# Performance work log

Hardware: AMD Instinct MI355X
Metric: run time of the kernel (lower is better)

Reference implementation:

```python
import jax, jax.numpy as jnp
import numpy as np

B, S, D_MODEL, N_HEADS, D_K, D_V = 2, 2048, 1024, 16, 64, 64


def setup_inputs() -> dict:
    key = jax.random.key(0)
    k1, k2, k3, k4, k5, k6, k7 = jax.random.split(key, 7)
    scale = 1.0 / np.sqrt(D_MODEL)
    inputs = {
        "input_Q": jax.random.normal(k1, (B, S, D_MODEL), dtype=jnp.float32),
        "input_K": jax.random.normal(k2, (B, S, D_MODEL), dtype=jnp.float32),
        "input_V": jax.random.normal(k3, (B, S, D_MODEL), dtype=jnp.float32),
        # causal mask: True means position is masked out (matches masked_fill_)
        "attn_mask": jnp.broadcast_to(
            ~jnp.tril(jnp.ones((S, S), dtype=bool)), (B, S, S)
        ),
        "flag": 0,
        "W_Q": jax.random.normal(k4, (D_MODEL, N_HEADS * D_K), dtype=jnp.float32) * scale,
        "W_K": jax.random.normal(k5, (D_MODEL, N_HEADS * D_K), dtype=jnp.float32) * scale,
        "W_V": jax.random.normal(k6, (D_MODEL, N_HEADS * D_V), dtype=jnp.float32) * scale,
        "W_O": jax.random.normal(k7, (N_HEADS * D_V, D_MODEL), dtype=jnp.float32) * scale,
    }
    return inputs


def reference(input_Q, input_K, input_V, attn_mask, flag, W_Q, W_K, W_V, W_O):
    b = input_Q.shape[0]
    # project and split heads: [b, h, s, d]
    Q = (input_Q @ W_Q).reshape(b, -1, N_HEADS, D_K).transpose(0, 2, 1, 3)
    K = (input_K @ W_K).reshape(b, -1, N_HEADS, D_K).transpose(0, 2, 1, 3)
    V = (input_V @ W_V).reshape(b, -1, N_HEADS, D_V).transpose(0, 2, 1, 3)
    # scaled dot-product attention with additive large-negative masking
    scores = jnp.einsum("bhqd,bhkd->bhqk", Q, K) / np.sqrt(D_K).astype(np.float32)
    scores = jnp.where(attn_mask[:, None, :, :], jnp.float32(-1e9), scores)
    attn = jax.nn.softmax(scores, axis=-1)
    context = jnp.einsum("bhqk,bhkd->bhqd", attn, V)  # [b, h, s, d_v]
    context = context.transpose(0, 2, 1, 3).reshape(b, -1, N_HEADS * D_V)
    return context @ W_O
```

## Files before the change

kernel.cpp:

```cpp
#include <hip/hip_runtime.h>

#define DEVINL __device__ __forceinline__

typedef __attribute__((ext_vector_type(8))) short short8;
typedef __attribute__((ext_vector_type(4))) short sh4;
typedef __attribute__((ext_vector_type(4))) float floatx4;

constexpr int S_LEN = 2048;
constexpr int DM    = 1024;
constexpr int NHEAD = 16;
constexpr int DHEAD = 64;
constexpr int BATCH = 2;
constexpr int MROWS = BATCH * S_LEN;
constexpr float LOG2E = 1.44269504f;
constexpr float SM_C1 = 0.125f * LOG2E;
constexpr float SM_C2 = -24.0f * LOG2E;

#define MFMA16(a, b, c) __builtin_amdgcn_mfma_f32_16x16x16bf16_1k(a, b, c, 0, 0, 0)

DEVINL unsigned short f2bf(float x) {
  union { float f; unsigned u; } un; un.f = x;
  unsigned u = un.u;
  return (unsigned short)((u + 0x7fffu + ((u >> 16) & 1u)) >> 16);
}
DEVINL unsigned short f2bf_fast(float x) {
  union { float f; unsigned u; } un; un.f = x;
  return (unsigned short)((un.u + 0x8000u) >> 16);
}

__global__ __launch_bounds__(256) void prep_kernel(const float* __restrict__ s0,
                                                   const float* __restrict__ s1,
                                                   const float* __restrict__ s2,
                                                   unsigned short* __restrict__ d0,
                                                   unsigned short* __restrict__ d1,
                                                   unsigned short* __restrict__ d2,
                                                   const float* __restrict__ W0,
                                                   const float* __restrict__ W1,
                                                   const float* __restrict__ W2,
                                                   const float* __restrict__ W3,
                                                   unsigned short* __restrict__ T0,
                                                   unsigned short* __restrict__ T1,
                                                   unsigned short* __restrict__ T2,
                                                   unsigned short* __restrict__ T3) {
  __shared__ unsigned short tile[32][33];
  const int y = blockIdx.y;
  if (y < 3) {
    const float* s = y == 0 ? s0 : (y == 1 ? s1 : s2);
    unsigned short* d = y == 0 ? d0 : (y == 1 ? d1 : d2);
    int i = (blockIdx.x * 256 + threadIdx.x) * 4;
    float4 v = *(const float4*)(s + i);
    unsigned lo = (unsigned)f2bf(v.x) | ((unsigned)f2bf(v.y) << 16);
    unsigned hi = (unsigned)f2bf(v.z) | ((unsigned)f2bf(v.w) << 16);
    *(uint2*)(d + i) = make_uint2(lo, hi);
  } else {
    const int x = blockIdx.x;
    const int wsel = x >> 10, rem = x & 1023;
    const float* W = wsel == 0 ? W0 : (wsel == 1 ? W1 : (wsel == 2 ? W2 : W3));
    unsigned short* Wt = wsel == 0 ? T0 : (wsel == 1 ? T1 : (wsel == 2 ? T2 : T3));
    int t = threadIdx.x;
    int c = t & 31, r0 = t >> 5;
    int nB = (rem & 31) * 32, kB = (rem >> 5) * 32;
    for (int i = 0; i < 4; ++i) {
      int r = r0 + i * 8;
      tile[r][c] = f2bf(W[(size_t)(kB + r) * DM + nB + c]);
    }
    __syncthreads();
    for (int i = 0; i < 4; ++i) {
      int r = r0 + i * 8;
      Wt[(size_t)(nB + r) * DM + kB + c] = tile[c][r];
    }
  }
}

DEVINL void load_lds16(const unsigned short* g, unsigned short* l) {
  __builtin_amdgcn_global_load_lds((const __attribute__((address_space(1))) unsigned int*)g,
                                   (__attribute__((address_space(3))) unsigned int*)l,
                                   16, 0, 0);
}

template <int MODE>
DEVINL void gemm_body(const unsigned short* __restrict__ A,
                      const unsigned short* __restrict__ Bt,
                      void* __restrict__ Cout) {
  constexpr int K = 1024, N = 1024;
  __shared__ alignas(16) unsigned short As[128 * 32];
  __shared__ alignas(16) unsigned short Bs[128 * 32];
  const int tid  = threadIdx.x;
  const int wave = tid >> 6, lane = tid & 63;
  const int quad = lane >> 4, l16 = lane & 15;
  const int mBase = blockIdx.y * 128, nBase = blockIdx.x * 128;
  const int wm = (wave >> 1) * 64, wn = (wave & 1) * 64;
  const int sr = lane >> 2;
  const int sc = (lane & 3) * 8;
  floatx4 acc[4][4] = {};

  for (int k0 = 0; k0 < K; k0 += 32) {
    __syncthreads();
#pragma unroll
    for (int j = 0; j < 2; ++j) {
      int row = wave * 32 + j * 16 + sr;
      load_lds16(A  + (size_t)(mBase + row) * K + k0 + sc, As + (wave * 32 + j * 16) * 32);
      load_lds16(Bt + (size_t)(nBase + row) * K + k0 + sc, Bs + (wave * 32 + j * 16) * 32);
    }
    __syncthreads();
    short8 af[4], bfr[4];
#pragma unroll
    for (int mt = 0; mt < 4; ++mt) af[mt]  = *(const short8*)&As[(wm + mt * 16 + l16) * 32 + quad * 8];
#pragma unroll
    for (int nt = 0; nt < 4; ++nt) bfr[nt] = *(const short8*)&Bs[(wn + nt * 16 + l16) * 32 + quad * 8];
#pragma unroll
    for (int mt = 0; mt < 4; ++mt)
#pragma unroll
      for (int nt = 0; nt < 4; ++nt)
        acc[mt][nt] = __builtin_amdgcn_mfma_f32_16x16x32_bf16(af[mt], bfr[nt], acc[mt][nt], 0, 0, 0);
  }

#pragma unroll
  for (int mt = 0; mt < 4; ++mt)
#pragma unroll
    for (int nt = 0; nt < 4; ++nt) {
      const int m = mBase + wm + mt * 16 + quad * 4;
      const int n = nBase + wn + nt * 16 + l16;
      if (MODE == 2) {
        const int bq = m >> 11, s = m & 2047;
        const int hh = n >> 6,  d = n & 63;
        unsigned short w4[4];
#pragma unroll
        for (int r = 0; r < 4; ++r) w4[r] = f2bf(acc[mt][nt][r]);
        *(uint2*)&((unsigned short*)Cout)[((size_t)((bq * 16 + hh) * 64 + d)) * S_LEN + s] =
            *(const uint2*)w4;
      } else {
#pragma unroll
        for (int r = 0; r < 4; ++r)
          ((unsigned short*)Cout)[(size_t)(m + r) * N + n] = f2bf(acc[mt][nt][r]);
      }
    }
}

__global__ __launch_bounds__(256) void gemm_qkv(const unsigned short* __restrict__ A0,
                                                const unsigned short* __restrict__ A1,
                                                const unsigned short* __restrict__ A2,
                                                const unsigned short* __restrict__ B0,
                                                const unsigned short* __restrict__ B1,
                                                const unsigned short* __restrict__ B2,
                                                unsigned short* __restrict__ C0,
                                                unsigned short* __restrict__ C1,
                                                unsigned short* __restrict__ C2) {
  const int z = blockIdx.z;
  if (z == 2)      gemm_body<2>(A2, B2, C2);
  else if (z == 1) gemm_body<0>(A1, B1, C1);
  else             gemm_body<0>(A0, B0, C0);
}

__global__ __launch_bounds__(256) void gemm_out64(const unsigned short* __restrict__ A,
                                                  const unsigned short* __restrict__ Bt,
                                                  float* __restrict__ C) {
  constexpr int K = 1024, N = 1024;
  __shared__ alignas(16) unsigned short As[64 * 32];
  __shared__ alignas(16) unsigned short Bs[128 * 32];
  const int tid  = threadIdx.x;
  const int wave = tid >> 6, lane = tid & 63;
  const int quad = lane >> 4, l16 = lane & 15;
  const int mBase = blockIdx.y * 64, nBase = blockIdx.x * 128;
  const int wm = (wave >> 1) * 32, wn = (wave & 1) * 64;
  const int sr = lane >> 2;
  const int sc = (lane & 3) * 8;
  floatx4 acc[2][4] = {};

  for (int k0 = 0; k0 < K; k0 += 32) {
    __syncthreads();
    load_lds16(A + (size_t)(mBase + wave * 16 + sr) * K + k0 + sc, As + (wave * 16) * 32);
#pragma unroll
    for (int j = 0; j < 2; ++j) {
      int row = wave * 32 + j * 16 + sr;
      load_lds16(Bt + (size_t)(nBase + row) * K + k0 + sc, Bs + (wave * 32 + j * 16) * 32);
    }
    __syncthreads();
    short8 af[2], bfr[4];
#pragma unroll
    for (int mt = 0; mt < 2; ++mt) af[mt]  = *(const short8*)&As[(wm + mt * 16 + l16) * 32 + quad * 8];
#pragma unroll
    for (int nt = 0; nt < 4; ++nt) bfr[nt] = *(const short8*)&Bs[(wn + nt * 16 + l16) * 32 + quad * 8];
#pragma unroll
    for (int mt = 0; mt < 2; ++mt)
#pragma unroll
      for (int nt = 0; nt < 4; ++nt)
        acc[mt][nt] = __builtin_amdgcn_mfma_f32_16x16x32_bf16(af[mt], bfr[nt], acc[mt][nt], 0, 0, 0);
  }

#pragma unroll
  for (int mt = 0; mt < 2; ++mt)
#pragma unroll
    for (int nt = 0; nt < 4; ++nt)
#pragma unroll
      for (int r = 0; r < 4; ++r) {
        int m = mBase + wm + mt * 16 + quad * 4 + r;
        int n = nBase + wn + nt * 16 + l16;
        C[(size_t)m * N + n] = acc[mt][nt][r];
      }
}

__global__ __launch_bounds__(256, 3) void attn_kernel(const unsigned short* __restrict__ Qp,
                                                      const unsigned short* __restrict__ Kp,
                                                      const unsigned short* __restrict__ Vtg,
                                                      unsigned short* __restrict__ ctx) {
  const int bh = blockIdx.y;
  const int b  = bh >> 4, h = bh & 15;
  const int tid = threadIdx.x;
  const int w = tid >> 6, lane = tid & 63;
  const int quad = lane >> 4, l16 = lane & 15;

  __shared__ alignas(16) unsigned short KVs[2 * 8192];
  __shared__ float rsL[4][4][16];
  __shared__ alignas(16) float Ored[4][4][16][20];

  const unsigned short* Kbh = Kp  + (size_t)(b * S_LEN) * DM + h * DHEAD;
  const unsigned short* Vbh = Vtg + (size_t)(bh * DHEAD) * S_LEN;

  int srow[4], scol[4];
#pragma unroll
  for (int j = 0; j < 4; ++j) {
    const int p = (w & 1) * 256 + j * 64 + lane;
    srow[j] = p >> 3;
    scol[j] = ((p & 7) ^ (srow[j] & 7)) * 8;
  }
  const bool stageK = (w < 2);

  const int swz = l16 & 7;
  const int kRow = (w * 16 + l16) * 64;
  const int kOff0 = kRow + ((0 + quad) ^ swz) * 8;
  const int kOff1 = kRow + ((4 + quad) ^ swz) * 8;
  int vOff[4];
#pragma unroll
  for (int dt = 0; dt < 4; ++dt) {
    const int ch = 2 * w + (quad >> 1);
    vOff[dt] = 4096 + (dt * 16 + l16) * 64 + (ch ^ swz) * 8 + (quad & 1) * 4;
  }

  {
    unsigned short* dst = KVs + w * 2048;
#pragma unroll
    for (int j = 0; j < 4; ++j) {
      const unsigned short* src = stageK
          ? Kbh + (size_t)srow[j] * DM + scol[j]
          : Vbh + (size_t)srow[j] * S_LEN + scol[j];
      load_lds16(src, dst + j * 512);
    }
  }

  int cur = 0;

#pragma unroll 1
  for (int half = 0; half < 2; ++half) {
    const int qt = half ? (int)blockIdx.x : 31 - (int)blockIdx.x;
    const int Q0 = qt * 64;
    const int nT = qt + 1;

    short8 qB[4][2];
#pragma unroll
    for (int nt = 0; nt < 4; ++nt) {
      const size_t qr = ((size_t)(b * S_LEN + Q0 + nt * 16 + l16)) * DM + h * DHEAD + quad * 8;
      qB[nt][0] = *(const short8*)&Qp[qr];
      qB[nt][1] = *(const short8*)&Qp[qr + 32];
    }

    floatx4 o[4][4] = {};
    float rs[4] = {0.f, 0.f, 0.f, 0.f};

#pragma unroll 1
    for (int t = 0; t < nT; ++t) {
      asm volatile("s_waitcnt vmcnt(0)" ::: "memory");
      __syncthreads();

      const unsigned short* buf = KVs + cur * 8192;
      short8 kc0 = *(const short8*)&buf[kOff0];
      short8 kc1 = *(const short8*)&buf[kOff1];
      sh4 vv[4];
#pragma unroll
      for (int dt = 0; dt < 4; ++dt) vv[dt] = *(const sh4*)&buf[vOff[dt]];

      {
        const int tn = (t + 1 < nT) ? t + 1 : 0;
        const int kb = tn * 64;
        unsigned short* dst = KVs + (cur ^ 1) * 8192 + w * 2048;
#pragma unroll
        for (int j = 0; j < 4; ++j) {
          const unsigned short* src = stageK
              ? Kbh + (size_t)(kb + srow[j]) * DM + scol[j]
              : Vbh + (size_t)srow[j] * S_LEN + kb + scol[j];
          load_lds16(src, dst + j * 512);
        }
      }

      const bool masked = (t == nT - 1);
      const int sbase = w * 16 + quad * 4;

#pragma unroll
      for (int nt = 0; nt < 4; ++nt) {
        floatx4 sc = {};
        sc = __builtin_amdgcn_mfma_f32_16x16x32_bf16(kc0, qB[nt][0], sc, 0, 0, 0);
        sc = __builtin_amdgcn_mfma_f32_16x16x32_bf16(kc1, qB[nt][1], sc, 0, 0, 0);
        const int qoff = nt * 16 + l16;
        sh4 pa;
        float acc = 0.f;
#pragma unroll
        for (int r = 0; r < 4; ++r) {
          float p = __builtin_amdgcn_exp2f(fmaf(sc[r], SM_C1, SM_C2));
          if (masked && (sbase + r > qoff)) p = 0.f;
          acc += p;
          pa[r] = (short)f2bf_fast(p);
        }
        rs[nt] += acc;
#pragma unroll
        for (int dt = 0; dt < 4; ++dt)
          o[nt][dt] = MFMA16(pa, vv[dt], o[nt][dt]);
      }

      cur ^= 1;
    }

#pragma unroll
    for (int nt = 0; nt < 4; ++nt) {
      rs[nt] += __shfl_xor(rs[nt], 16, 64);
      rs[nt] += __shfl_xor(rs[nt], 32, 64);
    }
    if (quad == 0) {
#pragma unroll
      for (int nt = 0; nt < 4; ++nt) rsL[w][nt][l16] = rs[nt];
    }

    for (int nt = 0; nt < 4; ++nt) {
      __syncthreads();
#pragma unroll
      for (int dt = 0; dt < 4; ++dt)
        *(floatx4*)&Ored[w][dt][l16][quad * 4] = o[nt][dt];
      __syncthreads();
      floatx4 acc = {};
#pragma unroll
      for (int w2 = 0; w2 < 4; ++w2) {
        floatx4 v = *(const floatx4*)&Ored[w2][w][l16][quad * 4];
#pragma unroll
        for (int j = 0; j < 4; ++j) acc[j] += v[j];
      }
#pragma unroll
      for (int j = 0; j < 4; ++j) {
        const int q16 = quad * 4 + j;
        float l = rsL[0][nt][q16] + rsL[1][nt][q16] + rsL[2][nt][q16] + rsL[3][nt][q16];
        const size_t row = (size_t)(b * S_LEN + Q0 + nt * 16 + q16);
        ctx[row * DM + h * DHEAD + w * 16 + l16] = f2bf(acc[j] / l);
      }
    }
  }
}

extern "C" void kernel_launch(void* const* d_in, const int* in_sizes, int n_in,
                              void* d_out, int out_size, void* d_ws, size_t ws_size,
                              hipStream_t stream) {
  const float* Xq = (const float*)d_in[0];
  const float* Xk = (const float*)d_in[1];
  const float* Xv = (const float*)d_in[2];
  const float* Wq = (const float*)d_in[5];
  const float* Wk = (const float*)d_in[6];
  const float* Wv = (const float*)d_in[7];
  const float* Wo = (const float*)d_in[8];
  float* out = (float*)d_out;

  char* ws = (char*)d_ws;
  constexpr size_t XBYTES = (size_t)MROWS * DM * 2;
  constexpr size_t WBYTES = (size_t)DM * DM * 2;
  unsigned short* xq_bf = (unsigned short*)(ws);
  unsigned short* xk_bf = (unsigned short*)(ws + XBYTES);
  unsigned short* xv_bf = (unsigned short*)(ws + 2 * XBYTES);
  unsigned short* wqt   = (unsigned short*)(ws + 3 * XBYTES);
  unsigned short* wkt   = (unsigned short*)(ws + 3 * XBYTES + WBYTES);
  unsigned short* wvt   = (unsigned short*)(ws + 3 * XBYTES + 2 * WBYTES);
  unsigned short* wot   = (unsigned short*)(ws + 3 * XBYTES + 3 * WBYTES);
  unsigned short* qp    = (unsigned short*)(ws + 3 * XBYTES + 4 * WBYTES);
  unsigned short* kp    = (unsigned short*)(ws + 4 * XBYTES + 4 * WBYTES);
  unsigned short* vt    = (unsigned short*)(ws + 5 * XBYTES + 4 * WBYTES);
  unsigned short* ctx   = xq_bf;

  prep_kernel<<<dim3(4096, 4), 256, 0, stream>>>(Xq, Xk, Xv, xq_bf, xk_bf, xv_bf,
                                                 Wq, Wk, Wv, Wo, wqt, wkt, wvt, wot);

  gemm_qkv<<<dim3(DM / 128, MROWS / 128, 3), 256, 0, stream>>>(
      xq_bf, xk_bf, xv_bf, wqt, wkt, wvt, qp, kp, vt);

  attn_kernel<<<dim3(16, BATCH * NHEAD), 256, 0, stream>>>(qp, kp, vt, ctx);

  gemm_out64<<<dim3(DM / 128, MROWS / 64), 256, 0, stream>>>(ctx, wot, out);
}
```

Before: 231.3 us.

## Split attention query tiles across two wave groups with 512-thread blocks

The attention kernel moves to 512 threads. Waves are split into 4 key-slice groups times 2 query groups, so each wave holds half the output accumulators and Q fragments, and K/V staging is spread across all 8 waves. The LDS buffers are unioned so the reduction scratch reuses the K/V buffer, and the prefetch of the next half's first tile is replaced by a restart per half. The aim is fewer registers per wave and more waves to hide latency, at the cost of an extra sync and lost cross-half prefetch overlap.

```diff
diff --git a/kernel.cpp b/kernel.cpp
--- a/kernel.cpp
+++ b/kernel.cpp
@@ -200,7 +200,7 @@
       }
 }
 
-__global__ __launch_bounds__(256, 3) void attn_kernel(const unsigned short* __restrict__ Qp,
+__global__ __launch_bounds__(512, 4) void attn_kernel(const unsigned short* __restrict__ Qp,
                                                       const unsigned short* __restrict__ Kp,
                                                       const unsigned short* __restrict__ Vtg,
                                                       unsigned short* __restrict__ ctx) {
@@ -209,46 +209,37 @@
   const int tid = threadIdx.x;
   const int w = tid >> 6, lane = tid & 63;
   const int quad = lane >> 4, l16 = lane & 15;
-
-  __shared__ alignas(16) unsigned short KVs[2 * 8192];
-  __shared__ float rsL[4][4][16];
-  __shared__ alignas(16) float Ored[4][4][16][20];
+  const int sgrp = w & 3, qgrp = w >> 2;
+
+  __shared__ alignas(16) char smem[41984];
+  unsigned short* KVs = (unsigned short*)smem;
+  float* OredB = (float*)smem;
+  float* rsLB  = (float*)(smem + 40960);
 
   const unsigned short* Kbh = Kp  + (size_t)(b * S_LEN) * DM + h * DHEAD;
   const unsigned short* Vbh = Vtg + (size_t)(bh * DHEAD) * S_LEN;
 
-  int srow[4], scol[4];
-#pragma unroll
-  for (int j = 0; j < 4; ++j) {
-    const int p = (w & 1) * 256 + j * 64 + lane;
+  const bool stageK = (w < 4);
+  const int vbase = stageK ? 0 : 4096;
+  int srow[2], scol[2];
+#pragma unroll
+  for (int j = 0; j < 2; ++j) {
+    const int p = sgrp * 128 + j * 64 + lane;
     srow[j] = p >> 3;
     scol[j] = ((p & 7) ^ (srow[j] & 7)) * 8;
   }
-  const bool stageK = (w < 2);
+  const int dstOff = vbase + sgrp * 1024;
 
   const int swz = l16 & 7;
-  const int kRow = (w * 16 + l16) * 64;
+  const int kRow = (sgrp * 16 + l16) * 64;
   const int kOff0 = kRow + ((0 + quad) ^ swz) * 8;
   const int kOff1 = kRow + ((4 + quad) ^ swz) * 8;
   int vOff[4];
 #pragma unroll
   for (int dt = 0; dt < 4; ++dt) {
-    const int ch = 2 * w + (quad >> 1);
+    const int ch = 2 * sgrp + (quad >> 1);
     vOff[dt] = 4096 + (dt * 16 + l16) * 64 + (ch ^ swz) * 8 + (quad & 1) * 4;
   }
-
-  {
-    unsigned short* dst = KVs + w * 2048;
-#pragma unroll
-    for (int j = 0; j < 4; ++j) {
-      const unsigned short* src = stageK
-          ? Kbh + (size_t)srow[j] * DM + scol[j]
-          : Vbh + (size_t)srow[j] * S_LEN + scol[j];
-      load_lds16(src, dst + j * 512);
-    }
-  }
-
-  int cur = 0;
 
 #pragma unroll 1
   for (int half = 0; half < 2; ++half) {
@@ -256,16 +247,30 @@
     const int Q0 = qt * 64;
     const int nT = qt + 1;
 
-    short8 qB[4][2];
-#pragma unroll
-    for (int nt = 0; nt < 4; ++nt) {
+    __syncthreads();
+    int cur = 0;
+    {
+      unsigned short* dst = KVs + dstOff;
+#pragma unroll
+      for (int j = 0; j < 2; ++j) {
+        const unsigned short* src = stageK
+            ? Kbh + (size_t)srow[j] * DM + scol[j]
+            : Vbh + (size_t)srow[j] * S_LEN + scol[j];
+        load_lds16(src, dst + j * 512);
+      }
+    }
+
+    short8 qB[2][2];
+#pragma unroll
+    for (int ntl = 0; ntl < 2; ++ntl) {
+      const int nt = qgrp * 2 + ntl;
       const size_t qr = ((size_t)(b * S_LEN + Q0 + nt * 16 + l16)) * DM + h * DHEAD + quad * 8;
-      qB[nt][0] = *(const short8*)&Qp[qr];
-      qB[nt][1] = *(const short8*)&Qp[qr + 32];
-    }
-
-    floatx4 o[4][4] = {};
-    float rs[4] = {0.f, 0.f, 0.f, 0.f};
+      qB[ntl][0] = *(const short8*)&Qp[qr];
+      qB[ntl][1] = *(const short8*)&Qp[qr + 32];
+    }
+
+    floatx4 o[2][4] = {};
+    float rs[2] = {0.f, 0.f};
 
 #pragma unroll 1
     for (int t = 0; t < nT; ++t) {
@@ -279,12 +284,11 @@
 #pragma unroll
       for (int dt = 0; dt < 4; ++dt) vv[dt] = *(const sh4*)&buf[vOff[dt]];
 
-      {
-        const int tn = (t + 1 < nT) ? t + 1 : 0;
-        const int kb = tn * 64;
-        unsigned short* dst = KVs + (cur ^ 1) * 8192 + w * 2048;
-#pragma unroll
-        for (int j = 0; j < 4; ++j) {
+      if (t + 1 < nT) {
+        const int kb = (t + 1) * 64;
+        unsigned short* dst = KVs + (cur ^ 1) * 8192 + dstOff;
+#pragma unroll
+        for (int j = 0; j < 2; ++j) {
           const unsigned short* src = stageK
               ? Kbh + (size_t)(kb + srow[j]) * DM + scol[j]
               : Vbh + (size_t)srow[j] * S_LEN + kb + scol[j];
@@ -293,13 +297,14 @@
       }
 
       const bool masked = (t == nT - 1);
-      const int sbase = w * 16 + quad * 4;
-
-#pragma unroll
-      for (int nt = 0; nt < 4; ++nt) {
+      const int sbase = sgrp * 16 + quad * 4;
+
+#pragma unroll
+      for (int ntl = 0; ntl < 2; ++ntl) {
+        const int nt = qgrp * 2 + ntl;
         floatx4 sc = {};
-        sc = __builtin_amdgcn_mfma_f32_16x16x32_bf16(kc0, qB[nt][0], sc, 0, 0, 0);
-        sc = __builtin_amdgcn_mfma_f32_16x16x32_bf16(kc1, qB[nt][1], sc, 0, 0, 0);
+        sc = __builtin_amdgcn_mfma_f32_16x16x32_bf16(kc0, qB[ntl][0], sc, 0, 0, 0);
+        sc = __builtin_amdgcn_mfma_f32_16x16x32_bf16(kc1, qB[ntl][1], sc, 0, 0, 0);
         const int qoff = nt * 16 + l16;
         sh4 pa;
         float acc = 0.f;
@@ -310,44 +315,50 @@
           acc += p;
           pa[r] = (short)f2bf_fast(p);
         }
-        rs[nt] += acc;
+        rs[ntl] += acc;
 #pragma unroll
         for (int dt = 0; dt < 4; ++dt)
-          o[nt][dt] = MFMA16(pa, vv[dt], o[nt][dt]);
+          o[ntl][dt] = MFMA16(pa, vv[dt], o[ntl][dt]);
       }
 
       cur ^= 1;
     }
 
 #pragma unroll
-    for (int nt = 0; nt < 4; ++nt) {
-      rs[nt] += __shfl_xor(rs[nt], 16, 64);
-      rs[nt] += __shfl_xor(rs[nt], 32, 64);
+    for (int ntl = 0; ntl < 2; ++ntl) {
+      rs[ntl] += __shfl_xor(rs[ntl], 16, 64);
+      rs[ntl] += __shfl_xor(rs[ntl], 32, 64);
     }
     if (quad == 0) {
 #pragma unroll
-      for (int nt = 0; nt < 4; ++nt) rsL[w][nt][l16] = rs[nt];
-    }
-
-    for (int nt = 0; nt < 4; ++nt) {
+      for (int ntl = 0; ntl < 2; ++ntl) rsLB[(w * 2 + ntl) * 16 + l16] = rs[ntl];
+    }
+
+#pragma unroll 1
+    for (int ntl = 0; ntl < 2; ++ntl) {
+      const int nt = qgrp * 2 + ntl;
       __syncthreads();
 #pragma unroll
       for (int dt = 0; dt < 4; ++dt)
-        *(floatx4*)&Ored[w][dt][l16][quad * 4] = o[nt][dt];
+        *(floatx4*)&OredB[((((qgrp * 4 + sgrp) * 4 + dt) * 16 + l16) * 20) + quad * 4] =
+            o[ntl][dt];
       __syncthreads();
       floatx4 acc = {};
 #pragma unroll
-      for (int w2 = 0; w2 < 4; ++w2) {
-        floatx4 v = *(const floatx4*)&Ored[w2][w][l16][quad * 4];
+      for (int s2 = 0; s2 < 4; ++s2) {
+        floatx4 v = *(const floatx4*)&OredB[((((qgrp * 4 + s2) * 4 + sgrp) * 16 + l16) * 20) + quad * 4];
 #pragma unroll
         for (int j = 0; j < 4; ++j) acc[j] += v[j];
       }
 #pragma unroll
       for (int j = 0; j < 4; ++j) {
         const int q16 = quad * 4 + j;
-        float l = rsL[0][nt][q16] + rsL[1][nt][q16] + rsL[2][nt][q16] + rsL[3][nt][q16];
+        float l = rsLB[((qgrp * 4 + 0) * 2 + ntl) * 16 + q16] +
+                  rsLB[((qgrp * 4 + 1) * 2 + ntl) * 16 + q16] +
+                  rsLB[((qgrp * 4 + 2) * 2 + ntl) * 16 + q16] +
+                  rsLB[((qgrp * 4 + 3) * 2 + ntl) * 16 + q16];
         const size_t row = (size_t)(b * S_LEN + Q0 + nt * 16 + q16);
-        ctx[row * DM + h * DHEAD + w * 16 + l16] = f2bf(acc[j] / l);
+        ctx[row * DM + h * DHEAD + sgrp * 16 + l16] = f2bf(acc[j] / l);
       }
     }
   }
@@ -386,7 +397,7 @@
   gemm_qkv<<<dim3(DM / 128, MROWS / 128, 3), 256, 0, stream>>>(
       xq_bf, xk_bf, xv_bf, wqt, wkt, wvt, qp, kp, vt);
 
-  attn_kernel<<<dim3(16, BATCH * NHEAD), 256, 0, stream>>>(qp, kp, vt, ctx);
+  attn_kernel<<<dim3(16, BATCH * NHEAD), 512, 0, stream>>>(qp, kp, vt, ctx);
 
   gemm_out64<<<dim3(DM / 128, MROWS / 64), 256, 0, stream>>>(ctx, wot, out);
 }
```

After: 470.2 us. +103.3%, slower.
